# Kernel tuning notes

Hardware: AMD Instinct MI355X
Metric: run time of the kernel (lower is better)

The kernel has to match this reference:

```python
import jax, jax.numpy as jnp
import numpy as np
from math import gcd


def _get_start_index(length):
    if length <= 2:
        return 0
    return (length - 1) // 2


def setup_inputs() -> dict:
    key = jax.random.key(0)
    k1, k2 = jax.random.split(key)
    N = 8388608          # signal length (2^23 samples)
    F = 1023             # FIR taps
    x = jax.random.normal(k1, (N,), dtype=jnp.float32)
    filter_coeffs = jax.random.normal(k2, (F,), dtype=jnp.float32)
    return {"x": x, "up": 3, "down": 2, "filter_coeffs": filter_coeffs}


def reference(x, up, down, filter_coeffs):
    # Reduce the rational ratio (static Python ints)
    g = gcd(up, down)
    up = up // g
    down = down // g

    N = x.shape[0]
    F = filter_coeffs.shape[0]

    # Zero-stuff: x_up[::up] = up * x  -> length up*N
    x_up = jnp.zeros(up * N, dtype=x.dtype).at[::up].set(up * x)

    start = _get_start_index(F)
    out_len = (N * up) // down + bool((N * up) % down)

    if up == 1 and down == 1:
        return x_up[:out_len]

    # torch.conv1d(x_up, flip(h), padding=F-1) == full convolution np.convolve(x_up, h)
    full = jnp.convolve(x_up, filter_coeffs, mode="full")  # length up*N + F - 1
    x_out = full[start::down]
    return x_out[:out_len]
```

## Files before the change

kernel.cpp:

```cpp
#include <hip/hip_runtime.h>


typedef __attribute__((ext_vector_type(8)))  short bf16x8;
typedef __attribute__((ext_vector_type(16))) float f32x16;

constexpr int SBLK   = 4096;
constexpr int NQ     = 26;
constexpr int NGROUP = 1073;
constexpr int LDSSEG = 1080;
constexpr int AFE    = NQ * 192;

__device__ __forceinline__ unsigned short f2bf_rne(float f) {
    union { float f; unsigned u; } c; c.f = f;
    return (unsigned short)((c.u + 0x7FFFu + ((c.u >> 16) & 1u)) >> 16);
}
__device__ __forceinline__ unsigned pk2(float a, float b) {
    unsigned ua = __builtin_bit_cast(unsigned, a) + 0x8000u;
    unsigned ub = __builtin_bit_cast(unsigned, b) + 0x8000u;
    return __builtin_amdgcn_perm(ub, ua, 0x07060302);
}
__device__ __forceinline__ int swz(int seg) { return seg ^ ((seg >> 3) & 7); }

__global__ __launch_bounds__(256)
void build_afr_kernel(const float* __restrict__ h, uint4* __restrict__ afr)
{
    const int e = blockIdx.x * 256 + threadIdx.x;
    if (e >= AFE) return;
    const int qq   = e / 192;
    const int rem  = e - qq * 192;
    const int r    = rem >> 6;
    const int lane = rem & 63;
    const int m    = lane & 31;
    const int hh   = lane >> 5;
    const int ub   = 16 * (qq + 2) - 2 * m + 8 * hh;
    unsigned w[4];
    #pragma unroll
    for (int jp = 0; jp < 4; ++jp) {
        unsigned short half[2];
        #pragma unroll
        for (int uu = 0; uu < 2; ++uu) {
            const int u   = ub + 2 * jp + uu;
            const int t   = 381 - u;
            const int hix = (r == 0) ? 3 * t - 2 : ((r == 1) ? 3 * t : 3 * t + 2);
            half[uu] = (t >= 0 && hix >= 0 && hix < 1023) ? f2bf_rne(3.0f * h[hix])
                                                          : (unsigned short)0;
        }
        w[jp] = (unsigned)half[0] | ((unsigned)half[1] << 16);
    }
    afr[e] = make_uint4(w[0], w[1], w[2], w[3]);
}

__global__ __launch_bounds__(256, 4)
void resample_mfma_kernel(const float* __restrict__ x,
                          const uint4* __restrict__ afr,
                          float* __restrict__ out, int N)
{
    __shared__ __align__(16) unsigned short xb[LDSSEG * 8];

    const int tid = threadIdx.x;
    const int s0  = blockIdx.x * SBLK;
    const int A0  = 2 * s0 - 212;
    char* lb = (char*)xb;

    for (int it = 0; it < 5; ++it) {
        const int g = tid + 256 * it;
        if (g >= NGROUP) break;
        const int gb = A0 + 8 * g;
        float f[8];
        if (gb >= 0 && gb + 7 < N) {
            const float4 lo = *reinterpret_cast<const float4*>(x + gb);
            const float4 hi = *reinterpret_cast<const float4*>(x + gb + 4);
            f[0]=lo.x; f[1]=lo.y; f[2]=lo.z; f[3]=lo.w;
            f[4]=hi.x; f[5]=hi.y; f[6]=hi.z; f[7]=hi.w;
        } else {
            #pragma unroll
            for (int e = 0; e < 8; ++e) {
                const int idx = gb + e;
                f[e] = (idx >= 0 && idx < N) ? x[idx] : 0.0f;
            }
        }
        const unsigned p01 = pk2(f[0], f[1]);
        const unsigned p23 = pk2(f[2], f[3]);
        const unsigned p45 = pk2(f[4], f[5]);
        const unsigned p67 = pk2(f[6], f[7]);
        *reinterpret_cast<unsigned*>(lb + 16 * swz(g) + 12)    = p01;
        *reinterpret_cast<uint2*>  (lb + 16 * swz(g + 1))      = make_uint2(p23, p45);
        *reinterpret_cast<unsigned*>(lb + 16 * swz(g + 1) + 8) = p67;
    }
    __syncthreads();

    const int wave = tid >> 6;
    const int lane = tid & 63;
    const int n    = lane & 31;
    const int hh   = lane >> 5;

    f32x16 acc[3] = {};

    const int segbase = 256 * wave + 8 * n + hh + 1;
    const uint4* ap = afr + lane;

    #pragma unroll
    for (int qq = 0; qq < NQ; ++qq) {
        const int seg = segbase + 2 * (qq + 2);
        const bf16x8 B = __builtin_bit_cast(
            bf16x8, *reinterpret_cast<const uint4*>(lb + 16 * swz(seg)));
        #pragma unroll
        for (int r = 0; r < 3; ++r) {
            const bf16x8 A = __builtin_bit_cast(bf16x8, ap[qq * 192 + r * 64]);
            acc[r] = __builtin_amdgcn_mfma_f32_32x32x16_bf16(A, B, acc[r], 0, 0, 0);
        }
    }

    float* ob = out + 3 * s0 + 3072 * wave + 12 * hh + 96 * n;
    #pragma unroll
    for (int c = 0; c < 4; ++c) {
        float* p = ob + 24 * c;
        *reinterpret_cast<float4*>(p) =
            make_float4(acc[0][4*c],   acc[1][4*c],   acc[2][4*c],   acc[0][4*c+1]);
        *reinterpret_cast<float4*>(p + 4) =
            make_float4(acc[1][4*c+1], acc[2][4*c+1], acc[0][4*c+2], acc[1][4*c+2]);
        *reinterpret_cast<float4*>(p + 8) =
            make_float4(acc[2][4*c+2], acc[0][4*c+3], acc[1][4*c+3], acc[2][4*c+3]);
    }
}

extern "C" void kernel_launch(void* const* d_in, const int* in_sizes, int n_in,
                              void* d_out, int out_size, void* d_ws, size_t ws_size,
                              hipStream_t stream)
{
    const float* x = (const float*)d_in[0];
    const float* h = (const float*)d_in[3];
    float* out = (float*)d_out;
    uint4* afr = (uint4*)d_ws;

    const int N    = in_sizes[0];
    const int S    = out_size / 3;
    const int nblk = S / SBLK;

    build_afr_kernel<<<(AFE + 255) / 256, 256, 0, stream>>>(h, afr);
    resample_mfma_kernel<<<nblk, 256, 0, stream>>>(x, afr, out, N);
}
```

Measured before the change: 113.5 us.

## Use single-wave blocks with private LDS tiles and batched global loads

Each block is now one 64-lane wave handling 1024 samples with its own small LDS halo tile, so the block-wide barrier goes away. All five float4 pairs are issued up front before packing into LDS, which raises memory-level parallelism. The MFMA loop now advances a filter-fragment pointer and is unrolled by 2 instead of fully, which lowers register pressure. The trade-off is more redundant halo loads per output (306 vs 1073/4 groups per wave) and four times as many blocks.

```diff
diff --git a/kernel.cpp b/kernel.cpp
--- a/kernel.cpp
+++ b/kernel.cpp
@@ -4,10 +4,9 @@
 typedef __attribute__((ext_vector_type(8)))  short bf16x8;
 typedef __attribute__((ext_vector_type(16))) float f32x16;
 
-constexpr int SBLK   = 4096;
 constexpr int NQ     = 26;
-constexpr int NGROUP = 1073;
-constexpr int LDSSEG = 1080;
+constexpr int NGROUP = 306;
+constexpr int LDSSEG = 312;
 constexpr int AFE    = NQ * 192;
 
 __device__ __forceinline__ unsigned short f2bf_rne(float f) {
@@ -50,68 +49,73 @@
     afr[e] = make_uint4(w[0], w[1], w[2], w[3]);
 }
 
-__global__ __launch_bounds__(256, 4)
+__global__ __launch_bounds__(64, 4)
 void resample_mfma_kernel(const float* __restrict__ x,
                           const uint4* __restrict__ afr,
                           float* __restrict__ out, int N)
 {
     __shared__ __align__(16) unsigned short xb[LDSSEG * 8];
-
-    const int tid = threadIdx.x;
-    const int s0  = blockIdx.x * SBLK;
-    const int A0  = 2 * s0 - 212;
     char* lb = (char*)xb;
 
-    for (int it = 0; it < 5; ++it) {
-        const int g = tid + 256 * it;
-        if (g >= NGROUP) break;
+    const int lane = threadIdx.x;
+    const int s0   = blockIdx.x * 1024;
+    const int A0   = 2 * s0 - 212;
+
+    float4 lo[5], hi[5];
+    #pragma unroll
+    for (int i = 0; i < 5; ++i) {
+        const int g  = lane + 64 * i;
         const int gb = A0 + 8 * g;
-        float f[8];
-        if (gb >= 0 && gb + 7 < N) {
-            const float4 lo = *reinterpret_cast<const float4*>(x + gb);
-            const float4 hi = *reinterpret_cast<const float4*>(x + gb + 4);
-            f[0]=lo.x; f[1]=lo.y; f[2]=lo.z; f[3]=lo.w;
-            f[4]=hi.x; f[5]=hi.y; f[6]=hi.z; f[7]=hi.w;
+        if (g < NGROUP && gb >= 0 && gb + 7 < N) {
+            lo[i] = *reinterpret_cast<const float4*>(x + gb);
+            hi[i] = *reinterpret_cast<const float4*>(x + gb + 4);
         } else {
+            float f[8];
             #pragma unroll
             for (int e = 0; e < 8; ++e) {
                 const int idx = gb + e;
-                f[e] = (idx >= 0 && idx < N) ? x[idx] : 0.0f;
+                f[e] = (g < NGROUP && idx >= 0 && idx < N) ? x[idx] : 0.0f;
             }
+            lo[i] = make_float4(f[0], f[1], f[2], f[3]);
+            hi[i] = make_float4(f[4], f[5], f[6], f[7]);
         }
-        const unsigned p01 = pk2(f[0], f[1]);
-        const unsigned p23 = pk2(f[2], f[3]);
-        const unsigned p45 = pk2(f[4], f[5]);
-        const unsigned p67 = pk2(f[6], f[7]);
+    }
+    #pragma unroll
+    for (int i = 0; i < 5; ++i) {
+        const int g = lane + 64 * i;
+        if (g >= NGROUP) continue;
+        const unsigned p01 = pk2(lo[i].x, lo[i].y);
+        const unsigned p23 = pk2(lo[i].z, lo[i].w);
+        const unsigned p45 = pk2(hi[i].x, hi[i].y);
+        const unsigned p67 = pk2(hi[i].z, hi[i].w);
         *reinterpret_cast<unsigned*>(lb + 16 * swz(g) + 12)    = p01;
         *reinterpret_cast<uint2*>  (lb + 16 * swz(g + 1))      = make_uint2(p23, p45);
         *reinterpret_cast<unsigned*>(lb + 16 * swz(g + 1) + 8) = p67;
     }
-    __syncthreads();
 
-    const int wave = tid >> 6;
-    const int lane = tid & 63;
-    const int n    = lane & 31;
-    const int hh   = lane >> 5;
+    const int n  = lane & 31;
+    const int hh = lane >> 5;
 
     f32x16 acc[3] = {};
 
-    const int segbase = 256 * wave + 8 * n + hh + 1;
-    const uint4* ap = afr + lane;
+    const int segbase  = 8 * n + hh + 1 + 4;
+    const uint4* aq = afr + lane;
 
-    #pragma unroll
+    #pragma unroll 2
     for (int qq = 0; qq < NQ; ++qq) {
-        const int seg = segbase + 2 * (qq + 2);
+        const int seg = segbase + 2 * qq;
         const bf16x8 B = __builtin_bit_cast(
             bf16x8, *reinterpret_cast<const uint4*>(lb + 16 * swz(seg)));
-        #pragma unroll
-        for (int r = 0; r < 3; ++r) {
-            const bf16x8 A = __builtin_bit_cast(bf16x8, ap[qq * 192 + r * 64]);
-            acc[r] = __builtin_amdgcn_mfma_f32_32x32x16_bf16(A, B, acc[r], 0, 0, 0);
-        }
+        const bf16x8 A0f = __builtin_bit_cast(bf16x8, aq[0]);
+        const bf16x8 A1f = __builtin_bit_cast(bf16x8, aq[64]);
+        const bf16x8 A2f = __builtin_bit_cast(bf16x8, aq[128]);
+        acc[0] = __builtin_amdgcn_mfma_f32_32x32x16_bf16(A0f, B, acc[0], 0, 0, 0);
+        acc[1] = __builtin_amdgcn_mfma_f32_32x32x16_bf16(A1f, B, acc[1], 0, 0, 0);
+        acc[2] = __builtin_amdgcn_mfma_f32_32x32x16_bf16(A2f, B, acc[2], 0, 0, 0);
+        aq += 192;
     }
 
-    float* ob = out + 3 * s0 + 3072 * wave + 12 * hh + 96 * n;
+    float* ob = out + 3 * s0 + 12 * hh + 96 * n;
     #pragma unroll
     for (int c = 0; c < 4; ++c) {
         float* p = ob + 24 * c;
@@ -135,8 +139,8 @@
 
     const int N    = in_sizes[0];
     const int S    = out_size / 3;
-    const int nblk = S / SBLK;
+    const int nblk = S / 1024;
 
     build_afr_kernel<<<(AFE + 255) / 256, 256, 0, stream>>>(h, afr);
-    resample_mfma_kernel<<<nblk, 256, 0, stream>>>(x, afr, out, N);
+    resample_mfma_kernel<<<nblk, 64, 0, stream>>>(x, afr, out, N);
 }
```

After: 111.6 us. About the same (-1.7%).
